# Performance work log

Hardware: AMD Instinct MI355X
Metric: run time of the kernel (lower is better)

Reference implementation:

```python
import jax, jax.numpy as jnp
import numpy as np

CD_COEFF = 1.0  # init_kwargs cd_coeff

def _chamfer(p1, p2):
    # p1: (B, N, 3), p2: (B, M, 3)
    # pairwise squared distances (B, N, M)
    d2 = jnp.sum((p1[:, :, None, :] - p2[:, None, :, :]) ** 2, axis=-1)
    d = jnp.sqrt(d2)  # L2 norm as in torch.norm(dist, 2, dim=3)
    min_nm = jnp.min(d, axis=2)  # (B, N): for each pred point, nearest target
    min_mn = jnp.min(d, axis=1)  # (B, M): for each target point, nearest pred
    # batch-normalized symmetric chamfer distance
    return jnp.mean(jnp.mean(min_nm, axis=1) + jnp.mean(min_mn, axis=1))

def setup_inputs() -> dict:
    key = jax.random.key(0)
    k1, k2 = jax.random.split(key)
    x_diff_pred = jax.random.normal(k1, (8, 4096, 3), dtype=jnp.float32)
    x_diff_target = jax.random.normal(k2, (8, 4096, 3), dtype=jnp.float32)
    return {"x_diff_pred": x_diff_pred, "x_diff_target": x_diff_target}

def reference(x_diff_pred, x_diff_target):
    cd = _chamfer(x_diff_pred, x_diff_target)
    loss = CD_COEFF * cd
    return loss
```

## Files before the change

kernel.cpp:

```cpp
#include <hip/hip_runtime.h>


typedef _Float16 f16x4 __attribute__((ext_vector_type(4)));
typedef _Float16 f16x8 __attribute__((ext_vector_type(8)));
typedef float    f32x16 __attribute__((ext_vector_type(16)));

#define BATCH 8
#define NPTS 4096
#define THREADS 512
#define WAVES 8
#define DBTILES (NPTS/32)
#define K1_BLOCKS 256

__device__ __forceinline__ float min3f(float a, float b, float c) {
    return fminf(fminf(a, b), c);
}

__global__ __launch_bounds__(THREADS, 2) void cd_mfma(
        const float* __restrict__ pred,
        const float* __restrict__ targ,
        float* __restrict__ Bsum) {
    __shared__ uint4 sdb[NPTS];
    __shared__ float wred[WAVES];
    const int bx   = blockIdx.x;
    const int tid  = threadIdx.x;
    const int dirb = bx >> 4;
    const int ctg  = bx & 15;
    const int wave = tid >> 6;
    const int lane = tid & 63;
    const int dir  = dirb >> 3;
    const int b    = dirb & 7;
    const float* Qraw = (dir ? targ : pred) + (size_t)b * NPTS * 3;
    const float* Draw = (dir ? pred : targ) + (size_t)b * NPTS * 3;

    for (int i = tid; i < NPTS; i += THREADS) {
        const float* p = Draw + (size_t)i * 3;
        _Float16 hx = (_Float16)p[0], hy = (_Float16)p[1], hz = (_Float16)p[2];
        float xr = (float)hx, yr = (float)hy, zr = (float)hz;
        float w  = fmaf(xr, xr, fmaf(yr, yr, zr * zr));
        _Float16 hhi = (_Float16)w;
        _Float16 hlo = (_Float16)(w - (float)hhi);
        f16x8 pkt = {hx, hy, hz, hhi, hlo, (_Float16)0.f, (_Float16)0.f, (_Float16)0.f};
        sdb[i] = __builtin_bit_cast(uint4, pkt);
    }

    const int q = (ctg * WAVES + wave) * 32 + (lane & 31);
    const float* qp = Qraw + (size_t)q * 3;
    _Float16 qhx = (_Float16)qp[0], qhy = (_Float16)qp[1], qhz = (_Float16)qp[2];
    float xr = (float)qhx, yr = (float)qhy, zr = (float)qhz;
    float nq = fmaf(xr, xr, fmaf(yr, yr, zr * zr));
    _Float16 mx = (_Float16)(-2.f * xr), my = (_Float16)(-2.f * yr),
             mz = (_Float16)(-2.f * zr), one = (_Float16)1.f, zz = (_Float16)0.f;
    f16x4 Bf = (lane < 32) ? (f16x4){mx, my, mz, one}
                           : (f16x4){one, zz, zz, zz};

    __syncthreads();

    const char* sb = (const char*)sdb;
    int off = (lane & 31) * 16 + ((lane >> 5) << 3);

    const f32x16 Z = {};
    const float inf = __uint_as_float(0x7F800000u);
    float m = inf;
    auto fold = [&](const f32x16& a) {
        float s0 = min3f(a[0],  a[1],  a[2]);
        float s1 = min3f(a[3],  a[4],  a[5]);
        float s2 = min3f(a[6],  a[7],  a[8]);
        float s3 = min3f(a[9],  a[10], a[11]);
        float s4 = min3f(a[12], a[13], a[14]);
        float t0 = min3f(s0, s1, s2);
        float t1 = min3f(s3, s4, a[15]);
        m = min3f(m, t0, t1);
    };
    auto rd = [&]() { f16x4 v = *(const f16x4*)(sb + off); off += 512; return v; };

    f32x16 acc0 = __builtin_amdgcn_mfma_f32_32x32x8f16(rd(), Bf, Z, 0, 0, 0);
    f32x16 acc1 = __builtin_amdgcn_mfma_f32_32x32x8f16(rd(), Bf, Z, 0, 0, 0);
    f32x16 acc2 = __builtin_amdgcn_mfma_f32_32x32x8f16(rd(), Bf, Z, 0, 0, 0);
    f32x16 acc3 = __builtin_amdgcn_mfma_f32_32x32x8f16(rd(), Bf, Z, 0, 0, 0);
    #pragma unroll 4
    for (int j = 4; j < DBTILES; j += 4) {
        fold(acc0); acc0 = __builtin_amdgcn_mfma_f32_32x32x8f16(rd(), Bf, Z, 0, 0, 0);
        fold(acc1); acc1 = __builtin_amdgcn_mfma_f32_32x32x8f16(rd(), Bf, Z, 0, 0, 0);
        fold(acc2); acc2 = __builtin_amdgcn_mfma_f32_32x32x8f16(rd(), Bf, Z, 0, 0, 0);
        fold(acc3); acc3 = __builtin_amdgcn_mfma_f32_32x32x8f16(rd(), Bf, Z, 0, 0, 0);
    }
    fold(acc0); fold(acc1); fold(acc2); fold(acc3);

    m = fminf(m, __shfl_xor(m, 32, 64));
    float d = sqrtf(fmaxf(m + nq, 0.f));
    d += __shfl_xor(d, 16, 64);
    d += __shfl_xor(d,  8, 64);
    d += __shfl_xor(d,  4, 64);
    d += __shfl_xor(d,  2, 64);
    d += __shfl_xor(d,  1, 64);
    if (lane == 0) wred[wave] = d;
    __syncthreads();
    if (tid == 0) {
        float s = ((wred[0] + wred[1]) + (wred[2] + wred[3]))
                + ((wred[4] + wred[5]) + (wred[6] + wred[7]));
        Bsum[bx] = s;
    }
}

__global__ __launch_bounds__(256) void cd_final(
        const float* __restrict__ Bsum, float* __restrict__ out) {
    const int tid = threadIdx.x;
    float s = Bsum[tid];
    __shared__ float red[256];
    red[tid] = s;
    __syncthreads();
    for (int off = 128; off > 0; off >>= 1) {
        if (tid < off) red[tid] += red[tid + off];
        __syncthreads();
    }
    if (tid == 0) out[0] = red[0] * (1.0f / (float)(BATCH * NPTS));
}

extern "C" void kernel_launch(void* const* d_in, const int* in_sizes, int n_in,
                              void* d_out, int out_size, void* d_ws, size_t ws_size,
                              hipStream_t stream) {
    const float* pred = (const float*)d_in[0];
    const float* targ = (const float*)d_in[1];
    float* Bsum = (float*)d_ws;
    float* out  = (float*)d_out;

    cd_mfma<<<K1_BLOCKS, THREADS, 0, stream>>>(pred, targ, Bsum);
    cd_final<<<1, 256, 0, stream>>>(Bsum, out);
}
```

Baseline: 15.29 us.

## Stage database points in two LDS halves to raise occupancy

Cuts the shared-memory point buffer in half and processes the database in two sequential halves, each with its own load and barrier. It also reduces in-flight MFMA accumulators from four to two and raises launch bounds to target more waves per SIMD. The goal is more resident blocks for latency hiding. In exchange it adds extra barriers, a serialized load-compute phase per half, and less MFMA/fold overlap within a wave.

```diff
diff --git a/kernel.cpp b/kernel.cpp
--- a/kernel.cpp
+++ b/kernel.cpp
@@ -9,18 +9,19 @@
 #define NPTS 4096
 #define THREADS 512
 #define WAVES 8
-#define DBTILES (NPTS/32)
+#define HALF_PTS 2048
+#define HALF_TILES (HALF_PTS/32)
 #define K1_BLOCKS 256
 
 __device__ __forceinline__ float min3f(float a, float b, float c) {
     return fminf(fminf(a, b), c);
 }
 
-__global__ __launch_bounds__(THREADS, 2) void cd_mfma(
+__global__ __launch_bounds__(THREADS, 8) void cd_mfma(
         const float* __restrict__ pred,
         const float* __restrict__ targ,
         float* __restrict__ Bsum) {
-    __shared__ uint4 sdb[NPTS];
+    __shared__ uint4 sdb[HALF_PTS];
     __shared__ float wred[WAVES];
     const int bx   = blockIdx.x;
     const int tid  = threadIdx.x;
@@ -33,17 +34,6 @@
     const float* Qraw = (dir ? targ : pred) + (size_t)b * NPTS * 3;
     const float* Draw = (dir ? pred : targ) + (size_t)b * NPTS * 3;
 
-    for (int i = tid; i < NPTS; i += THREADS) {
-        const float* p = Draw + (size_t)i * 3;
-        _Float16 hx = (_Float16)p[0], hy = (_Float16)p[1], hz = (_Float16)p[2];
-        float xr = (float)hx, yr = (float)hy, zr = (float)hz;
-        float w  = fmaf(xr, xr, fmaf(yr, yr, zr * zr));
-        _Float16 hhi = (_Float16)w;
-        _Float16 hlo = (_Float16)(w - (float)hhi);
-        f16x8 pkt = {hx, hy, hz, hhi, hlo, (_Float16)0.f, (_Float16)0.f, (_Float16)0.f};
-        sdb[i] = __builtin_bit_cast(uint4, pkt);
-    }
-
     const int q = (ctg * WAVES + wave) * 32 + (lane & 31);
     const float* qp = Qraw + (size_t)q * 3;
     _Float16 qhx = (_Float16)qp[0], qhy = (_Float16)qp[1], qhz = (_Float16)qp[2];
@@ -53,11 +43,6 @@
              mz = (_Float16)(-2.f * zr), one = (_Float16)1.f, zz = (_Float16)0.f;
     f16x4 Bf = (lane < 32) ? (f16x4){mx, my, mz, one}
                            : (f16x4){one, zz, zz, zz};
-
-    __syncthreads();
-
-    const char* sb = (const char*)sdb;
-    int off = (lane & 31) * 16 + ((lane >> 5) << 3);
 
     const f32x16 Z = {};
     const float inf = __uint_as_float(0x7F800000u);
@@ -72,20 +57,42 @@
         float t1 = min3f(s3, s4, a[15]);
         m = min3f(m, t0, t1);
     };
-    auto rd = [&]() { f16x4 v = *(const f16x4*)(sb + off); off += 512; return v; };
 
-    f32x16 acc0 = __builtin_amdgcn_mfma_f32_32x32x8f16(rd(), Bf, Z, 0, 0, 0);
-    f32x16 acc1 = __builtin_amdgcn_mfma_f32_32x32x8f16(rd(), Bf, Z, 0, 0, 0);
-    f32x16 acc2 = __builtin_amdgcn_mfma_f32_32x32x8f16(rd(), Bf, Z, 0, 0, 0);
-    f32x16 acc3 = __builtin_amdgcn_mfma_f32_32x32x8f16(rd(), Bf, Z, 0, 0, 0);
-    #pragma unroll 4
-    for (int j = 4; j < DBTILES; j += 4) {
-        fold(acc0); acc0 = __builtin_amdgcn_mfma_f32_32x32x8f16(rd(), Bf, Z, 0, 0, 0);
-        fold(acc1); acc1 = __builtin_amdgcn_mfma_f32_32x32x8f16(rd(), Bf, Z, 0, 0, 0);
-        fold(acc2); acc2 = __builtin_amdgcn_mfma_f32_32x32x8f16(rd(), Bf, Z, 0, 0, 0);
-        fold(acc3); acc3 = __builtin_amdgcn_mfma_f32_32x32x8f16(rd(), Bf, Z, 0, 0, 0);
+    const char* sb = (const char*)sdb;
+    const int off0 = (lane & 31) * 16 + ((lane >> 5) << 3);
+
+    #pragma unroll 1
+    for (int h = 0; h < 2; ++h) {
+        if (h) __syncthreads();
+
+        for (int i = tid; i < HALF_PTS; i += THREADS) {
+            const float* p = Draw + (size_t)(h * HALF_PTS + i) * 3;
+            _Float16 hx = (_Float16)p[0], hy = (_Float16)p[1], hz = (_Float16)p[2];
+            float xf = (float)hx, yf = (float)hy, zf = (float)hz;
+            float w  = fmaf(xf, xf, fmaf(yf, yf, zf * zf));
+            _Float16 hhi = (_Float16)w;
+            _Float16 hlo = (_Float16)(w - (float)hhi);
+            f16x8 pkt = {hx, hy, hz, hhi, hlo,
+                         (_Float16)0.f, (_Float16)0.f, (_Float16)0.f};
+            sdb[i] = __builtin_bit_cast(uint4, pkt);
+        }
+        __syncthreads();
+
+        int off = off0;
+        auto rd = [&]() { f16x4 v = *(const f16x4*)(sb + off); off += 512; return v; };
+        f32x16 acc0 = __builtin_amdgcn_mfma_f32_32x32x8f16(rd(), Bf, Z, 0, 0, 0);
+        f32x16 acc1 = __builtin_amdgcn_mfma_f32_32x32x8f16(rd(), Bf, Z, 0, 0, 0);
+        #pragma unroll 4
+        for (int j = 2; j < HALF_TILES; j += 2) {
+            fold(acc0);
+            acc0 = __builtin_amdgcn_mfma_f32_32x32x8f16(rd(), Bf, Z, 0, 0, 0);
+            fold(acc1);
+            acc1 = __builtin_amdgcn_mfma_f32_32x32x8f16(rd(), Bf, Z, 0, 0, 0);
+        }
+        fold(acc0);
+        fold(acc1);
+        __syncthreads();
     }
-    fold(acc0); fold(acc1); fold(acc2); fold(acc3);
 
     m = fminf(m, __shfl_xor(m, 32, 64));
     float d = sqrtf(fmaxf(m + nq, 0.f));
```

After: 15.81 us. +3.4%, slower.
